# Performance work log

Hardware: AMD Instinct MI355X
Metric: run time of the kernel (lower is better)

## Reference

```python
import jax, jax.numpy as jnp
import numpy as np

B, S, D = 2, 2048, 1024
H = 16
HD = D // H  # 64

def setup_inputs() -> dict:
    key = jax.random.key(0)
    k1, k2, k3 = jax.random.split(key, 3)
    scale = 0.02
    return {
        "x": jax.random.normal(k1, (B, S, D), dtype=jnp.float32),
        "w_qkv": jax.random.normal(k2, (D, 3 * D), dtype=jnp.float32) * scale,
        "b_qkv": jnp.zeros((3 * D,), dtype=jnp.float32),
        "w_proj": jax.random.normal(k3, (D, D), dtype=jnp.float32) * scale,
        "b_proj": jnp.zeros((D,), dtype=jnp.float32),
    }

def reference(x, w_qkv, b_qkv, w_proj, b_proj):
    batch, seq_len, _ = x.shape
    qkv = x @ w_qkv + b_qkv                      # [B,S,3D]
    qkv = qkv.reshape(batch, seq_len, 3, H, HD)
    qkv = jnp.transpose(qkv, (2, 0, 3, 1, 4))    # [3,B,H,S,HD]
    q, k, v = qkv[0], qkv[1], qkv[2]
    attn = jnp.einsum('bhqd,bhkd->bhqk', q, k) / jnp.sqrt(jnp.float32(HD))
    attn = jax.nn.softmax(attn, axis=-1)         # [B,H,S,S]
    out = jnp.einsum('bhqk,bhkd->bhqd', attn, v)
    out = jnp.transpose(out, (0, 2, 1, 3)).reshape(batch, seq_len, -1)
    return out @ w_proj + b_proj
```

## Files before the change

### kernel.cpp

```cpp
#include <hip/hip_runtime.h>
#include <math.h>

#define SS 2048
#define DD 1024
#define HH 16
#define NQKV 3072
#define MROWS 4096
#define KD 1024

typedef __attribute__((ext_vector_type(8))) short bf16x8;
typedef __attribute__((ext_vector_type(8))) unsigned short us8;
typedef __attribute__((ext_vector_type(4))) float f32x4;
typedef __attribute__((ext_vector_type(16))) float f32x16;
typedef unsigned short u16;
typedef unsigned int u32;

#define SCALE_C 0.18033688011112042f

#define GLDS16(g, l) \
  __builtin_amdgcn_global_load_lds((const __attribute__((address_space(1))) u32*)(g), \
                                   (__attribute__((address_space(3))) u32*)(l), 16, 0, 0)

static __device__ __forceinline__ u16 f2bf(float f) {
  union { float f; u32 u; } v; v.f = f;
  u32 u = v.u;
  u += 0x7fffu + ((u >> 16) & 1u);
  return (u16)(u >> 16);
}
static __device__ __forceinline__ u32 pk2(float a, float b) {
  return (u32)f2bf(a) | ((u32)f2bf(b) << 16);
}
static __device__ __forceinline__ u32 pk2t(float a, float b) {
  union { float f; u32 u; } ua, ub; ua.f = a; ub.f = b;
  return __builtin_amdgcn_perm(ub.u, ua.u, 0x07060302u);
}

__global__ __launch_bounds__(256) void k_prep(const float* __restrict__ x,
                                              const float* __restrict__ w_qkv,
                                              const float* __restrict__ w_proj,
                                              u16* __restrict__ x_bf,
                                              u16* __restrict__ wqkvT,
                                              u16* __restrict__ wprojT) {
  __shared__ float t[64][65];
  int bx = blockIdx.x;
  int tid = threadIdx.x;
  if (bx < 2048) {
    int i = (bx * 256 + tid) * 8;
    float4 a = *(const float4*)(x + i);
    float4 b = *(const float4*)(x + i + 4);
    us8 o;
    o[0] = f2bf(a.x); o[1] = f2bf(a.y); o[2] = f2bf(a.z); o[3] = f2bf(a.w);
    o[4] = f2bf(b.x); o[5] = f2bf(b.y); o[6] = f2bf(b.z); o[7] = f2bf(b.w);
    *(us8*)(x_bf + i) = o;
    return;
  }
  const float* in; u16* out; int R = KD, C, tile;
  if (bx < 2048 + 768) { in = w_qkv; out = wqkvT; C = NQKV; tile = bx - 2048; }
  else                 { in = w_proj; out = wprojT; C = DD; tile = bx - 2816; }
  int tilesC = C >> 6;
  int tc = tile % tilesC, tr = tile / tilesC;
  int r0 = tr * 64, c0 = tc * 64;
  int lx = tid & 63, ly = tid >> 6;
#pragma unroll
  for (int i = 0; i < 16; i++) {
    int rr = ly + i * 4;
    t[rr][lx] = in[(size_t)(r0 + rr) * C + c0 + lx];
  }
  __syncthreads();
#pragma unroll
  for (int i = 0; i < 16; i++) {
    int cc = ly + i * 4;
    out[(size_t)(c0 + cc) * R + r0 + lx] = f2bf(t[lx][cc]);
  }
}

template <int MODE, int BM>
__global__ __launch_bounds__(256, 2) void k_gemm(const u16* __restrict__ A,
                                                 const u16* __restrict__ Bt,
                                                 const float* __restrict__ bias,
                                                 void* __restrict__ Cout,
                                                 u16* __restrict__ vt,
                                                 int M, int N, int K) {
  constexpr int MT = BM / 32;
  __shared__ alignas(16) u16 As[BM * 64];
  __shared__ alignas(16) u16 Bs[128 * 64];
  const int tid = threadIdx.x;
  const int w = tid >> 6, ln = tid & 63;
  const int wm = w >> 1, wn = w & 1;
  const int lm = ln & 15, quad = ln >> 4;
  const int m0 = blockIdx.y * BM, n0 = blockIdx.x * 128;
  const int lr = ln >> 3, cc = ln & 7;
  const int cg = cc ^ lr;

  f32x4 acc[MT][4];
#pragma unroll
  for (int i = 0; i < MT; i++)
#pragma unroll
    for (int j = 0; j < 4; j++) acc[i][j] = (f32x4){0.f, 0.f, 0.f, 0.f};

  const u16* gA = A  + (size_t)(m0 + lr) * K + cg * 8;
  const u16* gB = Bt + (size_t)(n0 + lr) * K + cg * 8;

  for (int k0 = 0; k0 < K; k0 += 64) {
#pragma unroll
    for (int ii = 0; ii < MT; ii++) {
      int i = w + 4 * ii;
      GLDS16(gA + (size_t)(8 * i) * K + k0, (char*)As + i * 1024);
    }
#pragma unroll
    for (int ii = 0; ii < 4; ii++) {
      int i = w + 4 * ii;
      GLDS16(gB + (size_t)(8 * i) * K + k0, (char*)Bs + i * 1024);
    }
    __syncthreads();
    bf16x8 af[MT][2], bfr[4][2];
#pragma unroll
    for (int t = 0; t < MT; t++)
#pragma unroll
      for (int kk = 0; kk < 2; kk++)
        af[t][kk] = *(const bf16x8*)((const char*)As + (wm * (MT * 16) + t * 16 + lm) * 128 +
                                     (((kk * 4 + quad) ^ (lm & 7)) * 16));
#pragma unroll
    for (int t = 0; t < 4; t++)
#pragma unroll
      for (int kk = 0; kk < 2; kk++)
        bfr[t][kk] = *(const bf16x8*)((const char*)Bs + (wn * 64 + t * 16 + lm) * 128 +
                                      (((kk * 4 + quad) ^ (lm & 7)) * 16));
#pragma unroll
    for (int kk = 0; kk < 2; kk++)
#pragma unroll
      for (int mt = 0; mt < MT; mt++)
#pragma unroll
        for (int nt = 0; nt < 4; nt++)
          acc[mt][nt] = __builtin_amdgcn_mfma_f32_16x16x32_bf16(af[mt][kk], bfr[nt][kk], acc[mt][nt], 0, 0, 0);
    __syncthreads();
  }

  float bv[4];
#pragma unroll
  for (int nt = 0; nt < 4; nt++) bv[nt] = bias[n0 + wn * 64 + nt * 16 + lm];

  if (MODE == 2 && n0 >= 2 * DD) {
    int b = m0 >> 11;
    int s0 = (m0 & 2047) + wm * 64;
#pragma unroll
    for (int mt = 0; mt < MT; mt++) {
      int s = s0 + mt * 16 + quad * 4;
#pragma unroll
      for (int nt = 0; nt < 4; nt++) {
        int n = n0 + wn * 64 + nt * 16 + lm;
        int bh = b * HH + ((n - 2 * DD) >> 6);
        int d = n & 63;
        uint2 v;
        v.x = pk2(acc[mt][nt][0] + bv[nt], acc[mt][nt][1] + bv[nt]);
        v.y = pk2(acc[mt][nt][2] + bv[nt], acc[mt][nt][3] + bv[nt]);
        *(uint2*)&vt[(size_t)(bh * 64 + d) * SS + s] = v;
      }
    }
    return;
  }

  const float qs = (MODE == 2 && n0 < DD) ? SCALE_C : 1.0f;
#pragma unroll
  for (int mt = 0; mt < MT; mt++) {
#pragma unroll
    for (int r = 0; r < 4; r++) {
      int row = m0 + wm * (MT * 16) + mt * 16 + quad * 4 + r;
#pragma unroll
      for (int nt = 0; nt < 4; nt++) {
        int col = n0 + wn * 64 + nt * 16 + lm;
        float v = (acc[mt][nt][r] + bv[nt]) * qs;
        if (MODE == 2) ((u16*)Cout)[(size_t)row * N + col] = f2bf(v);
        else           ((float*)Cout)[(size_t)row * N + col] = v;
      }
    }
  }
}

__global__ __launch_bounds__(256, 2) void k_attn(const u16* __restrict__ qkv,
                                                 const u16* __restrict__ vt,
                                                 u16* __restrict__ attn) {
  __shared__ alignas(16) u16 Ks[2][128 * 64];
  __shared__ alignas(16) u16 Vs[2][64 * 128];

  const int tid = threadIdx.x;
  const int w = tid >> 6, ln = tid & 63;
  const int qn = ln & 31, h5 = ln >> 5;
  const int bx = blockIdx.x;
  const int bh = bx >> 4;
  const int q0 = (bx & 15) * 128;
  const int b = bh >> 4, h = bh & 15;
  const size_t qkv_b = (size_t)b * SS * NQKV;
  const int hcol = h * 64;

  const int lr = ln >> 3, cc = ln & 7;
  const int cg = cc ^ lr;
  const int vr = ln >> 4, c16 = ln & 15;

  bf16x8 qf[4];
  {
    const u16* qp = qkv + qkv_b + (size_t)(q0 + w * 32 + qn) * NQKV + hcol + h5 * 8;
#pragma unroll
    for (int ks = 0; ks < 4; ks++) qf[ks] = *(const bf16x8*)(qp + ks * 16);
  }

  f32x16 o[2];
#pragma unroll
  for (int i = 0; i < 16; i++) { o[0][i] = 0.f; o[1][i] = 0.f; }
  float lsum = 0.f;

#pragma unroll
  for (int rr = 0; rr < 4; rr++) {
    int i = w + 4 * rr;
    GLDS16(qkv + qkv_b + (size_t)(8 * i + lr) * NQKV + DD + hcol + cg * 8, (char*)Ks[0] + i * 1024);
    int cgv = c16 ^ ((4 * i + vr) & 15);
    GLDS16(vt + (size_t)(bh * 64 + 4 * i + vr) * SS + cgv * 8,             (char*)Vs[0] + i * 1024);
  }

#pragma unroll 1
  for (int it = 0; it < SS / 128; it++) {
    __syncthreads();

    if (it + 1 < SS / 128) {
      int kv1 = (it + 1) * 128;
      char* kd = (char*)Ks[(it + 1) & 1];
      char* vd = (char*)Vs[(it + 1) & 1];
#pragma unroll
      for (int rr = 0; rr < 4; rr++) {
        int i = w + 4 * rr;
        GLDS16(qkv + qkv_b + (size_t)(kv1 + 8 * i + lr) * NQKV + DD + hcol + cg * 8, kd + i * 1024);
        int cgv = c16 ^ ((4 * i + vr) & 15);
        GLDS16(vt + (size_t)(bh * 64 + 4 * i + vr) * SS + kv1 + cgv * 8,             vd + i * 1024);
      }
    }

    const char* ksb = (const char*)Ks[it & 1];
    const char* vsb = (const char*)Vs[it & 1];

#pragma unroll
    for (int sub = 0; sub < 2; sub++) {
      f32x16 s0, s1;
#pragma unroll
      for (int i = 0; i < 16; i++) { s0[i] = 0.f; s1[i] = 0.f; }
#pragma unroll
      for (int ks = 0; ks < 4; ks++) {
        int ch = 2 * ks + h5;
        bf16x8 kf0 = *(const bf16x8*)(ksb + (sub * 64 + qn) * 128 + ((ch ^ (qn & 7)) * 16));
        bf16x8 kf1 = *(const bf16x8*)(ksb + (sub * 64 + 32 + qn) * 128 + ((ch ^ (qn & 7)) * 16));
        s0 = __builtin_amdgcn_mfma_f32_32x32x16_bf16(kf0, qf[ks], s0, 0, 0, 0);
        s1 = __builtin_amdgcn_mfma_f32_32x32x16_bf16(kf1, qf[ks], s1, 0, 0, 0);
      }

      bf16x8 vf[2][4];
#pragma unroll
      for (int dm = 0; dm < 2; dm++)
#pragma unroll
        for (int ks2 = 0; ks2 < 4; ks2++) {
          int d = dm * 32 + qn;
          int ch16 = 8 * sub + 2 * ks2 + h5;
          vf[dm][ks2] = *(const bf16x8*)(vsb + d * 256 + ((ch16 ^ (qn & 15)) * 16));
        }

      u32 pk0[4][2], pk1[4][2];
      float sum = 0.f;
#pragma unroll
      for (int g = 0; g < 4; g++) {
        float a0 = __builtin_amdgcn_exp2f(s0[4 * g]);
        float a1 = __builtin_amdgcn_exp2f(s0[4 * g + 1]);
        float a2 = __builtin_amdgcn_exp2f(s0[4 * g + 2]);
        float a3 = __builtin_amdgcn_exp2f(s0[4 * g + 3]);
        float b0 = __builtin_amdgcn_exp2f(s1[4 * g]);
        float b1 = __builtin_amdgcn_exp2f(s1[4 * g + 1]);
        float b2 = __builtin_amdgcn_exp2f(s1[4 * g + 2]);
        float b3 = __builtin_amdgcn_exp2f(s1[4 * g + 3]);
        sum += ((a0 + a1) + (a2 + a3)) + ((b0 + b1) + (b2 + b3));
        pk0[g][0] = pk2t(a0, a1); pk0[g][1] = pk2t(a2, a3);
        pk1[g][0] = pk2t(b0, b1); pk1[g][1] = pk2t(b2, b3);
      }
      lsum += sum;

      bf16x8 pf[4];
#pragma unroll
      for (int blk = 0; blk < 2; blk++) {
#pragma unroll
        for (int ks = 0; ks < 2; ks++) {
          u32 e0 = blk ? pk1[2 * ks][0]     : pk0[2 * ks][0];
          u32 e1 = blk ? pk1[2 * ks][1]     : pk0[2 * ks][1];
          u32 o0 = blk ? pk1[2 * ks + 1][0] : pk0[2 * ks + 1][0];
          u32 o1 = blk ? pk1[2 * ks + 1][1] : pk0[2 * ks + 1][1];
          u32 s0v = h5 ? e0 : o0;
          u32 s1v = h5 ? e1 : o1;
          u32 r0 = (u32)__shfl_xor((int)s0v, 32);
          u32 r1 = (u32)__shfl_xor((int)s1v, 32);
          union { u32 u[4]; bf16x8 v; } f;
          f.u[0] = h5 ? r0 : e0;
          f.u[1] = h5 ? r1 : e1;
          f.u[2] = h5 ? o0 : r0;
          f.u[3] = h5 ? o1 : r1;
          pf[blk * 2 + ks] = f.v;
        }
      }

#pragma unroll
      for (int ks2 = 0; ks2 < 4; ks2++) {
        o[0] = __builtin_amdgcn_mfma_f32_32x32x16_bf16(vf[0][ks2], pf[ks2], o[0], 0, 0, 0);
        o[1] = __builtin_amdgcn_mfma_f32_32x32x16_bf16(vf[1][ks2], pf[ks2], o[1], 0, 0, 0);
      }
    }
  }

  lsum += __shfl_xor(lsum, 32);
  float il = 1.0f / lsum;
  int row = b * SS + q0 + w * 32 + qn;
#pragma unroll
  for (int dm = 0; dm < 2; dm++)
#pragma unroll
    for (int g = 0; g < 4; g++) {
      int d = dm * 32 + 8 * g + 4 * h5;
      uint2 v;
      v.x = pk2(o[dm][4 * g] * il, o[dm][4 * g + 1] * il);
      v.y = pk2(o[dm][4 * g + 2] * il, o[dm][4 * g + 3] * il);
      *(uint2*)&attn[(size_t)row * DD + hcol + d] = v;
    }
}

extern "C" void kernel_launch(void* const* d_in, const int* in_sizes, int n_in,
                              void* d_out, int out_size, void* d_ws, size_t ws_size,
                              hipStream_t stream) {
  const float* x      = (const float*)d_in[0];
  const float* w_qkv  = (const float*)d_in[1];
  const float* b_qkv  = (const float*)d_in[2];
  const float* w_proj = (const float*)d_in[3];
  const float* b_proj = (const float*)d_in[4];
  float* out = (float*)d_out;

  u16* ws     = (u16*)d_ws;
  u16* x_bf   = ws;
  u16* wqkvT  = x_bf   + (size_t)MROWS * KD;
  u16* wprojT = wqkvT  + (size_t)NQKV * KD;
  u16* qkv    = wprojT + (size_t)DD * KD;
  u16* attn   = qkv    + (size_t)MROWS * NQKV;
  u16* vt     = attn   + (size_t)MROWS * DD;

  k_prep<<<3072, 256, 0, stream>>>(x, w_qkv, w_proj, x_bf, wqkvT, wprojT);
  k_gemm<2, 128><<<dim3(NQKV / 128, MROWS / 128), 256, 0, stream>>>(x_bf, wqkvT, b_qkv, qkv, vt, MROWS, NQKV, KD);
  k_attn<<<2 * HH * (SS / 128), 256, 0, stream>>>(qkv, vt, attn);
  k_gemm<0, 64><<<dim3(DD / 128, MROWS / 64), 256, 0, stream>>>(attn, wprojT, b_proj, out, nullptr, MROWS, DD, KD);
}
```

Baseline: 177.5 us.

## Double-buffer GEMM LDS tiles with K=32 steps and prefetch next tile

Splits the GEMM LDS staging into two buffers of half-depth (K=32) tiles and issues the global-to-LDS loads for the next K step before computing on the current one. This is meant to overlap memory latency with MFMA work and drops one barrier per iteration. The swizzle changes to match the 64-byte rows, and launch bounds rise from 2 to 3 blocks per CU to raise occupancy. In exchange, each barrier now covers half as much compute, and the higher occupancy target limits registers.

```diff
diff --git a/kernel.cpp b/kernel.cpp
--- a/kernel.cpp
+++ b/kernel.cpp
@@ -75,22 +75,23 @@
 }
 
 template <int MODE, int BM>
-__global__ __launch_bounds__(256, 2) void k_gemm(const u16* __restrict__ A,
+__global__ __launch_bounds__(256, 3) void k_gemm(const u16* __restrict__ A,
                                                  const u16* __restrict__ Bt,
                                                  const float* __restrict__ bias,
                                                  void* __restrict__ Cout,
                                                  u16* __restrict__ vt,
                                                  int M, int N, int K) {
   constexpr int MT = BM / 32;
-  __shared__ alignas(16) u16 As[BM * 64];
-  __shared__ alignas(16) u16 Bs[128 * 64];
+  constexpr int AI = BM / 64;
+  __shared__ alignas(16) u16 As[2][BM * 32];
+  __shared__ alignas(16) u16 Bs[2][128 * 32];
   const int tid = threadIdx.x;
   const int w = tid >> 6, ln = tid & 63;
   const int wm = w >> 1, wn = w & 1;
   const int lm = ln & 15, quad = ln >> 4;
   const int m0 = blockIdx.y * BM, n0 = blockIdx.x * 128;
-  const int lr = ln >> 3, cc = ln & 7;
-  const int cg = cc ^ lr;
+  const int lr = ln >> 2, c = ln & 3;
+  const int cg = c ^ (lr & 3);
 
   f32x4 acc[MT][4];
 #pragma unroll
@@ -101,39 +102,50 @@
   const u16* gA = A  + (size_t)(m0 + lr) * K + cg * 8;
   const u16* gB = Bt + (size_t)(n0 + lr) * K + cg * 8;
 
-  for (int k0 = 0; k0 < K; k0 += 64) {
-#pragma unroll
-    for (int ii = 0; ii < MT; ii++) {
-      int i = w + 4 * ii;
-      GLDS16(gA + (size_t)(8 * i) * K + k0, (char*)As + i * 1024);
-    }
-#pragma unroll
-    for (int ii = 0; ii < 4; ii++) {
-      int i = w + 4 * ii;
-      GLDS16(gB + (size_t)(8 * i) * K + k0, (char*)Bs + i * 1024);
-    }
+#pragma unroll
+  for (int ii = 0; ii < AI; ii++) {
+    int i = w + 4 * ii;
+    GLDS16(gA + (size_t)(16 * i) * K, (char*)As[0] + i * 1024);
+  }
+#pragma unroll
+  for (int ii = 0; ii < 2; ii++) {
+    int i = w + 4 * ii;
+    GLDS16(gB + (size_t)(16 * i) * K, (char*)Bs[0] + i * 1024);
+  }
+
+  for (int k0 = 0; k0 < K; k0 += 32) {
     __syncthreads();
-    bf16x8 af[MT][2], bfr[4][2];
+
+    if (k0 + 32 < K) {
+      char* ad = (char*)As[((k0 >> 5) + 1) & 1];
+      char* bd = (char*)Bs[((k0 >> 5) + 1) & 1];
+#pragma unroll
+      for (int ii = 0; ii < AI; ii++) {
+        int i = w + 4 * ii;
+        GLDS16(gA + (size_t)(16 * i) * K + k0 + 32, ad + i * 1024);
+      }
+#pragma unroll
+      for (int ii = 0; ii < 2; ii++) {
+        int i = w + 4 * ii;
+        GLDS16(gB + (size_t)(16 * i) * K + k0 + 32, bd + i * 1024);
+      }
+    }
+
+    const char* asb = (const char*)As[(k0 >> 5) & 1];
+    const char* bsb = (const char*)Bs[(k0 >> 5) & 1];
+
+    bf16x8 af[MT], bfr[4];
 #pragma unroll
     for (int t = 0; t < MT; t++)
-#pragma unroll
-      for (int kk = 0; kk < 2; kk++)
-        af[t][kk] = *(const bf16x8*)((const char*)As + (wm * (MT * 16) + t * 16 + lm) * 128 +
-                                     (((kk * 4 + quad) ^ (lm & 7)) * 16));
+      af[t] = *(const bf16x8*)(asb + (wm * (MT * 16) + t * 16 + lm) * 64 + ((quad ^ (lm & 3)) * 16));
 #pragma unroll
     for (int t = 0; t < 4; t++)
-#pragma unroll
-      for (int kk = 0; kk < 2; kk++)
-        bfr[t][kk] = *(const bf16x8*)((const char*)Bs + (wn * 64 + t * 16 + lm) * 128 +
-                                      (((kk * 4 + quad) ^ (lm & 7)) * 16));
-#pragma unroll
-    for (int kk = 0; kk < 2; kk++)
-#pragma unroll
-      for (int mt = 0; mt < MT; mt++)
-#pragma unroll
-        for (int nt = 0; nt < 4; nt++)
-          acc[mt][nt] = __builtin_amdgcn_mfma_f32_16x16x32_bf16(af[mt][kk], bfr[nt][kk], acc[mt][nt], 0, 0, 0);
-    __syncthreads();
+      bfr[t] = *(const bf16x8*)(bsb + (wn * 64 + t * 16 + lm) * 64 + ((quad ^ (lm & 3)) * 16));
+#pragma unroll
+    for (int mt = 0; mt < MT; mt++)
+#pragma unroll
+      for (int nt = 0; nt < 4; nt++)
+        acc[mt][nt] = __builtin_amdgcn_mfma_f32_16x16x32_bf16(af[mt], bfr[nt], acc[mt][nt], 0, 0, 0);
   }
 
   float bv[4];
```

Result: slower. 186.8 us (+5.3%).
